# Kernel optimization log

Measured on AMD Instinct MI355X. Metric: run time of the kernel, lower is better.

Reference implementation:

```python
import jax, jax.numpy as jnp
import numpy as np

B, N, F, E, D, H, L = 4, 2048, 2, 16, 32, 4, 2
GRAPH_LAYERS = 3
FLOW_ITERS = 10
COST_C = 1.0        # quadratic cost: c*x^2, inv_derivative(y) = y/(2c)
BIG_NUMBER = 1e7


def setup_inputs():
    key = jax.random.key(0)
    ks = jax.random.split(key, 20)
    node_features = jax.random.normal(ks[0], (B, N, F), jnp.float32)
    node_embeddings = jax.random.normal(ks[1], (B, N, E), jnp.float32)
    demands = jax.random.normal(ks[2], (B, N, 1), jnp.float32)
    demands = demands - demands.mean(axis=1, keepdims=True)  # flow conservation
    adj = (jax.random.uniform(ks[3], (B, N, N)) < 0.01).astype(jnp.float32)
    adj = adj * (1.0 - jnp.eye(N, dtype=jnp.float32))
    eye = jnp.broadcast_to(jnp.eye(N, dtype=jnp.float32), (B, N, N))
    neighborhoods = jnp.stack([eye, adj], axis=1)  # [B,L,N,N] hop-0 and hop-1
    def g(k, shape):
        return jax.random.normal(k, shape, jnp.float32) * 0.1
    params = {
        'We1': g(ks[4], (E + F, D)), 'be1': jnp.zeros((D,), jnp.float32),
        'We2': g(ks[5], (D, D)), 'be2': jnp.zeros((D,), jnp.float32),
        'w_attn': g(ks[6], (H, D)),
        'Wo': g(ks[7], (D, D)), 'bo': jnp.zeros((D,), jnp.float32),
        'Wz': g(ks[8], (D, D)), 'Uz': g(ks[9], (D, D)), 'bz': jnp.zeros((D,), jnp.float32),
        'Wr': g(ks[10], (D, D)), 'Ur': g(ks[11], (D, D)), 'br': jnp.zeros((D,), jnp.float32),
        'Wh': g(ks[12], (D, D)), 'Uh': g(ks[13], (D, D)), 'bh': jnp.zeros((D,), jnp.float32),
        'Wd1': g(ks[14], (D, D)), 'bd1': jnp.zeros((D,), jnp.float32),
        'Wd2': g(ks[15], (D, 1)), 'bd2': jnp.zeros((1,), jnp.float32),
        'Wv1': g(ks[16], (D, D)), 'bv1': jnp.zeros((D,), jnp.float32),
        'Wv2': g(ks[17], (D, 1)), 'bv2': jnp.zeros((1,), jnp.float32),
    }
    return {'node_features': node_features, 'node_embeddings': node_embeddings,
            'demands': demands, 'adj': adj, 'neighborhoods': neighborhoods, **params}


def _forward(node_features, node_embeddings, demands, adj, neighborhoods,
             We1, be1, We2, be2, w_attn, Wo, bo,
             Wz, Uz, bz, Wr, Ur, br, Wh, Uh, bh,
             Wd1, bd1, Wd2, bd2, Wv1, bv1, Wv2, bv2):
    # --- node encoder MLP (tanh, activate_final=True) ---
    x = jnp.concatenate([node_embeddings, node_features], axis=-1)   # [B,N,E+F]
    enc = jnp.tanh(jnp.tanh(x @ We1 + be1) @ We2 + be2)               # [B,N,D]
    # row-normalized neighborhood operators (degree-normalized aggregation)
    Mnorm = neighborhoods / (jnp.sum(neighborhoods, axis=-1, keepdims=True) + 1.0)
    # --- graph_layers x (attention neighborhood + GRU state update) ---
    for _ in range(GRAPH_LAYERS):
        agg = jnp.einsum('blnm,bmd->blnd', Mnorm, enc)                # [B,L,N,D]
        scores = jnp.einsum('blnd,hd->bhnl', jnp.tanh(agg), w_attn)   # [B,H,N,L]
        alpha = jax.nn.softmax(scores, axis=-1)
        ctx = jnp.einsum('bhnl,blnd->bnd', alpha, agg) / H            # mean over heads
        nbr = jnp.tanh(ctx @ Wo + bo)                                 # [B,N,D]
        z = jax.nn.sigmoid(nbr @ Wz + enc @ Uz + bz)
        r = jax.nn.sigmoid(nbr @ Wr + enc @ Ur + br)
        h = jnp.tanh(nbr @ Wh + (r * enc) @ Uh + bh)
        enc = z * enc + (1.0 - z) * h
    # --- primal: edge weights, masked softmax, proportional flow solver ---
    pred = (enc @ Wd1 + bd1) @ Wd2 + bd2                              # [B,N,1]
    pw = pred * jnp.transpose(pred, (0, 2, 1))                        # [B,N,N]
    weights = -BIG_NUMBER * (1.0 - adj) + pw
    fwp = jax.nn.softmax(weights, axis=-1)                            # rows sum to 1
    flow0 = fwp * jax.nn.relu(-demands)

    def step(flow, _):
        inflow = jnp.sum(flow, axis=1)[..., None]                     # [B,N,1]
        return fwp * jax.nn.relu(inflow - demands), None

    flow, _ = jax.lax.scan(step, flow0, None, length=FLOW_ITERS)
    flow_cost = jnp.sum(COST_C * flow * flow, axis=(1, 2))            # [B]
    # --- dual: dual variables, dual flows via inverse cost derivative ---
    dual = (enc @ Wv1 + bv1) @ Wv2 + bv2                              # [B,N,1]
    dd = dual - jnp.transpose(dual, (0, 2, 1))                        # [B,N,N]
    df = adj * jax.nn.relu(dd / (2.0 * COST_C))
    dual_cost = jnp.sum(COST_C * df * df - dd * df, axis=(1, 2)) \
        - jnp.sum(dual * demands, axis=(1, 2))                        # [B]
    return flow_cost - dual_cost                                      # primal-dual gap loss, [B]


def reference(node_features, node_embeddings, demands, adj, neighborhoods,
              We1, be1, We2, be2, w_attn, Wo, bo,
              Wz, Uz, bz, Wr, Ur, br, Wh, Uh, bh,
              Wd1, bd1, Wd2, bd2, Wv1, bv1, Wv2, bv2):
    return _forward(node_features, node_embeddings, demands, adj, neighborhoods,
                    We1, be1, We2, be2, w_attn, Wo, bo,
                    Wz, Uz, bz, Wr, Ur, br, Wh, Uh, bh,
                    Wd1, bd1, Wd2, bd2, Wv1, bv1, Wv2, bv2)
```

## Files before the change

### kernel.cpp

```cpp
#include <hip/hip_runtime.h>

#define NN 2048
#define NB 4
#define BN (NB * NN)
#define MAXD 96

__global__ __launch_bounds__(256) void k_front(
    const float* __restrict__ feat, const float* __restrict__ emb,
    const float* __restrict__ We1, const float* __restrict__ be1,
    const float* __restrict__ We2, const float* __restrict__ be2,
    float* __restrict__ enc_out,
    const float* __restrict__ adj, int* __restrict__ deg, int* __restrict__ cols,
    int* __restrict__ tdeg)
{
    int tid = threadIdx.x;
    if (blockIdx.x < 1024) {
        __shared__ float sW1[18 * 32], sb1[32], sW2[32 * 32], sb2[32];
        for (int i = tid; i < 18 * 32; i += 256) sW1[i] = We1[i];
        for (int i = tid; i < 32 * 32; i += 256) sW2[i] = We2[i];
        if (tid < 32) { sb1[tid] = be1[tid]; sb2[tid] = be2[tid]; }
        __syncthreads();
        int group = tid >> 5, j = tid & 31;
        int node = blockIdx.x * 8 + group;
        float x;
        if (j < 16)      x = emb[node * 16 + j];
        else if (j < 18) x = feat[node * 2 + (j - 16)];
        else             x = 0.f;
        float acc = sb1[j];
#pragma unroll
        for (int k = 0; k < 18; k++)
            acc += __shfl(x, k, 32) * sW1[k * 32 + j];
        float h = tanhf(acc);
        float acc2 = sb2[j];
#pragma unroll
        for (int k = 0; k < 32; k++)
            acc2 += __shfl(h, k, 32) * sW2[k * 32 + j];
        enc_out[node * 32 + j] = tanhf(acc2);
    } else {
        int wave = tid >> 6, lane = tid & 63;
        int row = (blockIdx.x - 1024) * 4 + wave;
        const float4* p = (const float4*)(adj + (size_t)row * NN);
        int cnt = 0;
        int base = row * MAXD;
#pragma unroll
        for (int it = 0; it < 8; it++) {
            float4 v = p[it * 64 + lane];
            float va[4] = { v.x, v.y, v.z, v.w };
#pragma unroll
            for (int c = 0; c < 4; c++) {
                unsigned long long m = __ballot(va[c] != 0.f);
                if (va[c] != 0.f) {
                    int pos = cnt + __popcll(m & ((1ull << lane) - 1ull));
                    if (pos < MAXD) cols[base + pos] = it * 256 + lane * 4 + c;
                }
                cnt += __popcll(m);
            }
        }
        if (lane == 0) {
            deg[row] = cnt < MAXD ? cnt : MAXD;
            tdeg[row] = 0;
        }
    }
}

__global__ __launch_bounds__(256) void k_layer(
    const float* __restrict__ enc_in, float* __restrict__ enc_out,
    const int* __restrict__ deg, const int* __restrict__ cols,
    const float* __restrict__ w_attn,
    const float* __restrict__ Wo, const float* __restrict__ bo,
    const float* __restrict__ Wz, const float* __restrict__ Uz, const float* __restrict__ bz,
    const float* __restrict__ Wr, const float* __restrict__ Ur, const float* __restrict__ br,
    const float* __restrict__ Wh, const float* __restrict__ Uh, const float* __restrict__ bh)
{
    __shared__ float sWo[1024], sWz[1024], sUz[1024], sWr[1024], sUr[1024], sWh[1024], sUh[1024];
    __shared__ float sbo[32], sbz[32], sbr[32], sbh[32], sAttn[128];
    int tid = threadIdx.x;
    for (int i = tid; i < 1024; i += 256) {
        sWo[i] = Wo[i]; sWz[i] = Wz[i]; sUz[i] = Uz[i];
        sWr[i] = Wr[i]; sUr[i] = Ur[i]; sWh[i] = Wh[i]; sUh[i] = Uh[i];
    }
    if (tid < 32) { sbo[tid] = bo[tid]; sbz[tid] = bz[tid]; sbr[tid] = br[tid]; sbh[tid] = bh[tid]; }
    if (tid < 128) sAttn[tid] = w_attn[tid];
    __syncthreads();
    int group = tid >> 5, j = tid & 31;
    int node = blockIdx.x * 8 + group;
    int b = node >> 11;
    const float* encB = enc_in + (size_t)(b * NN) * 32;
    float e = enc_in[node * 32 + j];
    float agg0 = 0.5f * e;
    int d = deg[node];
    const int* cp = cols + node * MAXD;
    int iA = cp[j];
    int iB = cp[j + 32];
    float a1 = 0.f, a1b = 0.f;
    int dmin = d < 32 ? d : 32;
#pragma unroll 4
    for (int i = 0; i < dmin - 1; i += 2) {
        int m0 = __shfl(iA, i, 32);
        int m1 = __shfl(iA, i + 1, 32);
        a1  += encB[m0 * 32 + j];
        a1b += encB[m1 * 32 + j];
    }
    if (dmin & 1) { int m = __shfl(iA, dmin - 1, 32); a1 += encB[m * 32 + j]; }
#pragma unroll 2
    for (int i = 32; i < d; i++) {
        int m = __shfl(iB, i - 32, 32);
        a1 += encB[m * 32 + j];
    }
    a1 = (a1 + a1b) * (1.0f / (float)(d + 1));
    float t0 = tanhf(agg0), t1 = tanhf(a1);
    float sc[8];
#pragma unroll
    for (int h2 = 0; h2 < 4; h2++) { sc[h2] = sAttn[h2 * 32 + j] * t0; sc[4 + h2] = sAttn[h2 * 32 + j] * t1; }
#pragma unroll
    for (int off = 16; off >= 1; off >>= 1)
#pragma unroll
        for (int q = 0; q < 8; q++) sc[q] += __shfl_xor(sc[q], off, 32);
    float c0 = 0.f, c1 = 0.f;
#pragma unroll
    for (int h2 = 0; h2 < 4; h2++) {
        float a = sc[h2], bsc = sc[4 + h2];
        float mx = fmaxf(a, bsc);
        float e0 = expf(a - mx), e1 = expf(bsc - mx);
        float inv = 1.0f / (e0 + e1);
        c0 += e0 * inv; c1 += e1 * inv;
    }
    c0 *= 0.25f; c1 *= 0.25f;
    float ctx = c0 * agg0 + c1 * a1;
    float acc = sbo[j];
#pragma unroll
    for (int k = 0; k < 32; k++) acc += __shfl(ctx, k, 32) * sWo[k * 32 + j];
    float nbr = tanhf(acc);
    float az = sbz[j], ar = sbr[j], ah = sbh[j];
#pragma unroll
    for (int k = 0; k < 32; k++) {
        float nb = __shfl(nbr, k, 32);
        float en = __shfl(e, k, 32);
        az += nb * sWz[k * 32 + j] + en * sUz[k * 32 + j];
        ar += nb * sWr[k * 32 + j] + en * sUr[k * 32 + j];
        ah += nb * sWh[k * 32 + j];
    }
    float z = 1.0f / (1.0f + expf(-az));
    float r = 1.0f / (1.0f + expf(-ar));
    float re = r * e;
#pragma unroll
    for (int k = 0; k < 32; k++) ah += __shfl(re, k, 32) * sUh[k * 32 + j];
    float hc = tanhf(ah);
    enc_out[node * 32 + j] = z * e + (1.0f - z) * hc;
}

__global__ __launch_bounds__(256) void k_heads(
    const float* __restrict__ enc,
    const float* __restrict__ Wd1, const float* __restrict__ bd1,
    const float* __restrict__ Wd2, const float* __restrict__ bd2,
    const float* __restrict__ Wv1, const float* __restrict__ bv1,
    const float* __restrict__ Wv2, const float* __restrict__ bv2,
    float* __restrict__ pred, float* __restrict__ dual)
{
    __shared__ float sWd1[1024], sWv1[1024], sbd1[32], sbv1[32], sWd2[32], sWv2[32];
    int tid = threadIdx.x;
    for (int i = tid; i < 1024; i += 256) { sWd1[i] = Wd1[i]; sWv1[i] = Wv1[i]; }
    if (tid < 32) { sbd1[tid] = bd1[tid]; sbv1[tid] = bv1[tid]; sWd2[tid] = Wd2[tid]; sWv2[tid] = Wv2[tid]; }
    __syncthreads();
    int group = tid >> 5, j = tid & 31;
    int node = blockIdx.x * 8 + group;
    float e = enc[node * 32 + j];
    float ad = sbd1[j], av = sbv1[j];
#pragma unroll
    for (int k = 0; k < 32; k++) {
        float en = __shfl(e, k, 32);
        ad += en * sWd1[k * 32 + j];
        av += en * sWv1[k * 32 + j];
    }
    float pd = ad * sWd2[j];
    float dv = av * sWv2[j];
#pragma unroll
    for (int off = 16; off >= 1; off >>= 1) {
        pd += __shfl_xor(pd, off, 32);
        dv += __shfl_xor(dv, off, 32);
    }
    if (j == 0) {
        pred[node] = pd + bd2[0];
        dual[node] = dv + bv2[0];
    }
}

__global__ __launch_bounds__(256) void k_edge_scatter(
    const int* __restrict__ deg, const int* __restrict__ cols,
    const float* __restrict__ pred, const float* __restrict__ dual,
    int* __restrict__ tdeg, float2* __restrict__ pk,
    float* __restrict__ rowsq, float* __restrict__ rowdual)
{
    int wave = threadIdx.x >> 6, lane = threadIdx.x & 63;
    int row = blockIdx.x * 4 + wave;
    int b = row >> 11;
    int rloc = row & (NN - 1);
    const float* predB = pred + b * NN;
    const float* dualB = dual + b * NN;
    int d = deg[row];
    int base = row * MAXD;
    float pn = pred[row];
    float dn = dual[row];
    float mx = -1e30f;
    for (int i = lane; i < d; i += 64) {
        int c = cols[base + i];
        mx = fmaxf(mx, pn * predB[c]);
    }
#pragma unroll
    for (int off = 32; off >= 1; off >>= 1) mx = fmaxf(mx, __shfl_xor(mx, off));
    float den = 0.f, du = 0.f;
    for (int i = lane; i < d; i += 64) {
        int c = cols[base + i];
        den += expf(pn * predB[c] - mx);
        float dd = dn - dualB[c];
        if (dd > 0.f) du -= 0.25f * dd * dd;
    }
#pragma unroll
    for (int off = 32; off >= 1; off >>= 1) { den += __shfl_xor(den, off); du += __shfl_xor(du, off); }
    float invden = 1.0f / den;
    float rs = 0.f;
    for (int i = lane; i < d; i += 64) {
        int c = cols[base + i];
        float f = expf(pn * predB[c] - mx) * invden;
        rs += f * f;
        int pos = atomicAdd(&tdeg[b * NN + c], 1);
        if (pos < MAXD) {
            pk[((size_t)(b * NN) + c) * MAXD + pos] = make_float2(f, __int_as_float(rloc));
        }
    }
#pragma unroll
    for (int off = 32; off >= 1; off >>= 1) rs += __shfl_xor(rs, off);
    if (lane == 0) { rowsq[row] = rs; rowdual[row] = du; }
}

#define FLOW_GATHER(EPTR, PAIRS, REM, DTOT, SRC, ACC_A, ACC_B)                     \
    {                                                                              \
        int i_ = 0;                                                                \
        for (; i_ + 1 < (PAIRS); i_ += 2) {                                        \
            float4 qa_ = (EPTR)[i_];                                               \
            float4 qb_ = (EPTR)[i_ + 1];                                           \
            ACC_A += qa_.x * SRC[__float_as_int(qa_.y)];                           \
            ACC_B += qa_.z * SRC[__float_as_int(qa_.w)];                           \
            ACC_A += qb_.x * SRC[__float_as_int(qb_.y)];                           \
            ACC_B += qb_.z * SRC[__float_as_int(qb_.w)];                           \
        }                                                                          \
        if (i_ < (PAIRS)) {                                                        \
            float4 q_ = (EPTR)[i_];                                                \
            ACC_A += q_.x * SRC[__float_as_int(q_.y)];                             \
            ACC_B += q_.z * SRC[__float_as_int(q_.w)];                             \
        }                                                                          \
        if (REM) {                                                                 \
            float2 q_ = ((const float2*)(EPTR))[(DTOT) - 1];                       \
            ACC_A += q_.x * SRC[__float_as_int(q_.y)];                             \
        }                                                                          \
    }

__global__ __launch_bounds__(1024) void k_flow_batch(
    const int* __restrict__ tdeg, const float2* __restrict__ pk,
    const float* __restrict__ demands,
    const float* __restrict__ rowsq, const float* __restrict__ rowdual,
    const float* __restrict__ dual, float* __restrict__ out)
{
    __shared__ float sdem[NN], sA[NN], sBuf[NN];
    __shared__ float red[3][16];
    int tid = threadIdx.x;
    int b = blockIdx.x;
    const float* demB = demands + b * NN;
    for (int n = tid; n < NN; n += 1024) {
        float dm = demB[n];
        sdem[n] = dm;
        sA[n] = fmaxf(-dm, 0.f);
    }
    __syncthreads();
    int n0 = tid, n1 = tid + 1024;
    int d0 = tdeg[b * NN + n0];
    int d1 = tdeg[b * NN + n1];
    const float4* e0 = (const float4*)(pk + ((size_t)(b * NN) + n0) * MAXD);
    const float4* e1 = (const float4*)(pk + ((size_t)(b * NN) + n1) * MAXD);
    int p0 = d0 >> 1, r0 = d0 & 1;
    int p1 = d1 >> 1, r1 = d1 & 1;
    float dm0 = sdem[n0], dm1 = sdem[n1];
#pragma unroll 1
    for (int it = 0; it < 5; it++) {
        {
            float a0 = 0.f, a0b = 0.f, a1 = 0.f, a1b = 0.f;
            FLOW_GATHER(e0, p0, r0, d0, sA, a0, a0b);
            FLOW_GATHER(e1, p1, r1, d1, sA, a1, a1b);
            sBuf[n0] = fmaxf(a0 + a0b - dm0, 0.f);
            sBuf[n1] = fmaxf(a1 + a1b - dm1, 0.f);
        }
        __syncthreads();
        {
            float a0 = 0.f, a0b = 0.f, a1 = 0.f, a1b = 0.f;
            FLOW_GATHER(e0, p0, r0, d0, sBuf, a0, a0b);
            FLOW_GATHER(e1, p1, r1, d1, sBuf, a1, a1b);
            sA[n0] = fmaxf(a0 + a0b - dm0, 0.f);
            sA[n1] = fmaxf(a1 + a1b - dm1, 0.f);
        }
        __syncthreads();
    }
    float fc = 0.f, ds = 0.f, dq = 0.f;
    for (int n = tid; n < NN; n += 1024) {
        int row = b * NN + n;
        float sv = sA[n];
        fc += rowsq[row] * sv * sv;
        ds += rowdual[row];
        dq += dual[row] * sdem[n];
    }
#pragma unroll
    for (int off = 32; off >= 1; off >>= 1) {
        fc += __shfl_xor(fc, off);
        ds += __shfl_xor(ds, off);
        dq += __shfl_xor(dq, off);
    }
    int wv = tid >> 6;
    if ((tid & 63) == 0) { red[0][wv] = fc; red[1][wv] = ds; red[2][wv] = dq; }
    __syncthreads();
    if (tid == 0) {
        float a = 0.f, s1 = 0.f, s2 = 0.f;
        for (int w = 0; w < 16; w++) { a += red[0][w]; s1 += red[1][w]; s2 += red[2][w]; }
        out[b] = a - s1 + s2;
    }
}

extern "C" void kernel_launch(void* const* d_in, const int* in_sizes, int n_in,
                              void* d_out, int out_size, void* d_ws, size_t ws_size,
                              hipStream_t stream) {
    const float* feat = (const float*)d_in[0];
    const float* emb  = (const float*)d_in[1];
    const float* dem  = (const float*)d_in[2];
    const float* adj  = (const float*)d_in[3];
    const float* We1 = (const float*)d_in[5];
    const float* be1 = (const float*)d_in[6];
    const float* We2 = (const float*)d_in[7];
    const float* be2 = (const float*)d_in[8];
    const float* w_attn = (const float*)d_in[9];
    const float* Wo = (const float*)d_in[10];
    const float* bo = (const float*)d_in[11];
    const float* Wz = (const float*)d_in[12];
    const float* Uz = (const float*)d_in[13];
    const float* bz = (const float*)d_in[14];
    const float* Wr = (const float*)d_in[15];
    const float* Ur = (const float*)d_in[16];
    const float* br = (const float*)d_in[17];
    const float* Wh = (const float*)d_in[18];
    const float* Uh = (const float*)d_in[19];
    const float* bh = (const float*)d_in[20];
    const float* Wd1 = (const float*)d_in[21];
    const float* bd1 = (const float*)d_in[22];
    const float* Wd2 = (const float*)d_in[23];
    const float* bd2 = (const float*)d_in[24];
    const float* Wv1 = (const float*)d_in[25];
    const float* bv1 = (const float*)d_in[26];
    const float* Wv2 = (const float*)d_in[27];
    const float* bv2 = (const float*)d_in[28];
    float* out = (float*)d_out;

    float* w = (float*)d_ws;
    float* enc0 = w;            w += (size_t)BN * 32;
    float* enc1 = w;            w += (size_t)BN * 32;
    int*   degp = (int*)w;      w += BN;
    int*   colp = (int*)w;      w += (size_t)BN * MAXD;
    float* pred = w;            w += BN;
    float* dual = w;            w += BN;
    float* rowsq = w;           w += BN;
    float* rowdual = w;         w += BN;
    int*   tdeg = (int*)w;      w += BN;
    float2* pk = (float2*)w;    w += (size_t)BN * MAXD * 2;

    k_front<<<3072, 256, 0, stream>>>(feat, emb, We1, be1, We2, be2, enc0,
                                      adj, degp, colp, tdeg);
    k_layer<<<BN / 8, 256, 0, stream>>>(enc0, enc1, degp, colp, w_attn,
                                        Wo, bo, Wz, Uz, bz, Wr, Ur, br, Wh, Uh, bh);
    k_layer<<<BN / 8, 256, 0, stream>>>(enc1, enc0, degp, colp, w_attn,
                                        Wo, bo, Wz, Uz, bz, Wr, Ur, br, Wh, Uh, bh);
    k_layer<<<BN / 8, 256, 0, stream>>>(enc0, enc1, degp, colp, w_attn,
                                        Wo, bo, Wz, Uz, bz, Wr, Ur, br, Wh, Uh, bh);
    k_heads<<<BN / 8, 256, 0, stream>>>(enc1, Wd1, bd1, Wd2, bd2, Wv1, bv1, Wv2, bv2,
                                        pred, dual);
    k_edge_scatter<<<BN / 4, 256, 0, stream>>>(degp, colp, pred, dual,
                                               tdeg, pk, rowsq, rowdual);
    k_flow_batch<<<NB, 1024, 0, stream>>>(tdeg, pk, dem,
                                          rowsq, rowdual, dual, out);
}
```

Baseline: 476.3 us.

## Transpose flow edge buffer to slot-major layout and enlarge layer blocks

New measurement: 435.9 us. -8.5%, faster.

```diff
diff --git a/kernel.cpp b/kernel.cpp
--- a/kernel.cpp
+++ b/kernel.cpp
@@ -63,7 +63,7 @@
     }
 }
 
-__global__ __launch_bounds__(256) void k_layer(
+__global__ __launch_bounds__(1024) void k_layer(
     const float* __restrict__ enc_in, float* __restrict__ enc_out,
     const int* __restrict__ deg, const int* __restrict__ cols,
     const float* __restrict__ w_attn,
@@ -75,7 +75,8 @@
     __shared__ float sWo[1024], sWz[1024], sUz[1024], sWr[1024], sUr[1024], sWh[1024], sUh[1024];
     __shared__ float sbo[32], sbz[32], sbr[32], sbh[32], sAttn[128];
     int tid = threadIdx.x;
-    for (int i = tid; i < 1024; i += 256) {
+    {
+        int i = tid;
         sWo[i] = Wo[i]; sWz[i] = Wz[i]; sUz[i] = Uz[i];
         sWr[i] = Wr[i]; sUr[i] = Ur[i]; sWh[i] = Wh[i]; sUh[i] = Uh[i];
     }
@@ -83,7 +84,7 @@
     if (tid < 128) sAttn[tid] = w_attn[tid];
     __syncthreads();
     int group = tid >> 5, j = tid & 31;
-    int node = blockIdx.x * 8 + group;
+    int node = blockIdx.x * 32 + group;
     int b = node >> 11;
     const float* encB = enc_in + (size_t)(b * NN) * 32;
     float e = enc_in[node * 32 + j];
@@ -225,35 +226,13 @@
         rs += f * f;
         int pos = atomicAdd(&tdeg[b * NN + c], 1);
         if (pos < MAXD) {
-            pk[((size_t)(b * NN) + c) * MAXD + pos] = make_float2(f, __int_as_float(rloc));
+            pk[(size_t)(b * MAXD + pos) * NN + c] = make_float2(f, __int_as_float(rloc));
         }
     }
 #pragma unroll
     for (int off = 32; off >= 1; off >>= 1) rs += __shfl_xor(rs, off);
     if (lane == 0) { rowsq[row] = rs; rowdual[row] = du; }
 }
-
-#define FLOW_GATHER(EPTR, PAIRS, REM, DTOT, SRC, ACC_A, ACC_B)                     \
-    {                                                                              \
-        int i_ = 0;                                                                \
-        for (; i_ + 1 < (PAIRS); i_ += 2) {                                        \
-            float4 qa_ = (EPTR)[i_];                                               \
-            float4 qb_ = (EPTR)[i_ + 1];                                           \
-            ACC_A += qa_.x * SRC[__float_as_int(qa_.y)];                           \
-            ACC_B += qa_.z * SRC[__float_as_int(qa_.w)];                           \
-            ACC_A += qb_.x * SRC[__float_as_int(qb_.y)];                           \
-            ACC_B += qb_.z * SRC[__float_as_int(qb_.w)];                           \
-        }                                                                          \
-        if (i_ < (PAIRS)) {                                                        \
-            float4 q_ = (EPTR)[i_];                                                \
-            ACC_A += q_.x * SRC[__float_as_int(q_.y)];                             \
-            ACC_B += q_.z * SRC[__float_as_int(q_.w)];                             \
-        }                                                                          \
-        if (REM) {                                                                 \
-            float2 q_ = ((const float2*)(EPTR))[(DTOT) - 1];                       \
-            ACC_A += q_.x * SRC[__float_as_int(q_.y)];                             \
-        }                                                                          \
-    }
 
 __global__ __launch_bounds__(1024) void k_flow_batch(
     const int* __restrict__ tdeg, const float2* __restrict__ pk,
@@ -275,25 +254,55 @@
     int n0 = tid, n1 = tid + 1024;
     int d0 = tdeg[b * NN + n0];
     int d1 = tdeg[b * NN + n1];
-    const float4* e0 = (const float4*)(pk + ((size_t)(b * NN) + n0) * MAXD);
-    const float4* e1 = (const float4*)(pk + ((size_t)(b * NN) + n1) * MAXD);
-    int p0 = d0 >> 1, r0 = d0 & 1;
-    int p1 = d1 >> 1, r1 = d1 & 1;
+    const float2* e0 = pk + (size_t)b * MAXD * NN + n0;
+    const float2* e1 = pk + (size_t)b * MAXD * NN + n1;
     float dm0 = sdem[n0], dm1 = sdem[n1];
 #pragma unroll 1
     for (int it = 0; it < 5; it++) {
         {
             float a0 = 0.f, a0b = 0.f, a1 = 0.f, a1b = 0.f;
-            FLOW_GATHER(e0, p0, r0, d0, sA, a0, a0b);
-            FLOW_GATHER(e1, p1, r1, d1, sA, a1, a1b);
+            int i = 0;
+#pragma unroll 2
+            for (; i + 1 < d0; i += 2) {
+                float2 qa = e0[(size_t)i * NN];
+                float2 qb = e0[(size_t)(i + 1) * NN];
+                a0  += qa.x * sA[__float_as_int(qa.y)];
+                a0b += qb.x * sA[__float_as_int(qb.y)];
+            }
+            if (i < d0) { float2 q = e0[(size_t)i * NN]; a0 += q.x * sA[__float_as_int(q.y)]; }
+            i = 0;
+#pragma unroll 2
+            for (; i + 1 < d1; i += 2) {
+                float2 qa = e1[(size_t)i * NN];
+                float2 qb = e1[(size_t)(i + 1) * NN];
+                a1  += qa.x * sA[__float_as_int(qa.y)];
+                a1b += qb.x * sA[__float_as_int(qb.y)];
+            }
+            if (i < d1) { float2 q = e1[(size_t)i * NN]; a1 += q.x * sA[__float_as_int(q.y)]; }
             sBuf[n0] = fmaxf(a0 + a0b - dm0, 0.f);
             sBuf[n1] = fmaxf(a1 + a1b - dm1, 0.f);
         }
         __syncthreads();
         {
             float a0 = 0.f, a0b = 0.f, a1 = 0.f, a1b = 0.f;
-            FLOW_GATHER(e0, p0, r0, d0, sBuf, a0, a0b);
-            FLOW_GATHER(e1, p1, r1, d1, sBuf, a1, a1b);
+            int i = 0;
+#pragma unroll 2
+            for (; i + 1 < d0; i += 2) {
+                float2 qa = e0[(size_t)i * NN];
+                float2 qb = e0[(size_t)(i + 1) * NN];
+                a0  += qa.x * sBuf[__float_as_int(qa.y)];
+                a0b += qb.x * sBuf[__float_as_int(qb.y)];
+            }
+            if (i < d0) { float2 q = e0[(size_t)i * NN]; a0 += q.x * sBuf[__float_as_int(q.y)]; }
+            i = 0;
+#pragma unroll 2
+            for (; i + 1 < d1; i += 2) {
+                float2 qa = e1[(size_t)i * NN];
+                float2 qb = e1[(size_t)(i + 1) * NN];
+                a1  += qa.x * sBuf[__float_as_int(qa.y)];
+                a1b += qb.x * sBuf[__float_as_int(qb.y)];
+            }
+            if (i < d1) { float2 q = e1[(size_t)i * NN]; a1 += q.x * sBuf[__float_as_int(q.y)]; }
             sA[n0] = fmaxf(a0 + a0b - dm0, 0.f);
             sA[n1] = fmaxf(a1 + a1b - dm1, 0.f);
         }
@@ -370,12 +379,12 @@
 
     k_front<<<3072, 256, 0, stream>>>(feat, emb, We1, be1, We2, be2, enc0,
                                       adj, degp, colp, tdeg);
-    k_layer<<<BN / 8, 256, 0, stream>>>(enc0, enc1, degp, colp, w_attn,
-                                        Wo, bo, Wz, Uz, bz, Wr, Ur, br, Wh, Uh, bh);
-    k_layer<<<BN / 8, 256, 0, stream>>>(enc1, enc0, degp, colp, w_attn,
-                                        Wo, bo, Wz, Uz, bz, Wr, Ur, br, Wh, Uh, bh);
-    k_layer<<<BN / 8, 256, 0, stream>>>(enc0, enc1, degp, colp, w_attn,
-                                        Wo, bo, Wz, Uz, bz, Wr, Ur, br, Wh, Uh, bh);
+    k_layer<<<BN / 32, 1024, 0, stream>>>(enc0, enc1, degp, colp, w_attn,
+                                          Wo, bo, Wz, Uz, bz, Wr, Ur, br, Wh, Uh, bh);
+    k_layer<<<BN / 32, 1024, 0, stream>>>(enc1, enc0, degp, colp, w_attn,
+                                          Wo, bo, Wz, Uz, bz, Wr, Ur, br, Wh, Uh, bh);
+    k_layer<<<BN / 32, 1024, 0, stream>>>(enc0, enc1, degp, colp, w_attn,
+                                          Wo, bo, Wz, Uz, bz, Wr, Ur, br, Wh, Uh, bh);
     k_heads<<<BN / 8, 256, 0, stream>>>(enc1, Wd1, bd1, Wd2, bd2, Wv1, bv1, Wv2, bv2,
                                         pred, dual);
     k_edge_scatter<<<BN / 4, 256, 0, stream>>>(degp, colp, pred, dual,
```

## Store transposed flow edges column-major and widen layer blocks to 1024 threads

Applied to the files above, without the earlier changes.

Measured after the change: 456.6 us. 4.1% less time.

```diff
diff --git a/kernel.cpp b/kernel.cpp
--- a/kernel.cpp
+++ b/kernel.cpp
@@ -63,7 +63,7 @@
     }
 }
 
-__global__ __launch_bounds__(256) void k_layer(
+__global__ __launch_bounds__(1024) void k_layer(
     const float* __restrict__ enc_in, float* __restrict__ enc_out,
     const int* __restrict__ deg, const int* __restrict__ cols,
     const float* __restrict__ w_attn,
@@ -75,7 +75,8 @@
     __shared__ float sWo[1024], sWz[1024], sUz[1024], sWr[1024], sUr[1024], sWh[1024], sUh[1024];
     __shared__ float sbo[32], sbz[32], sbr[32], sbh[32], sAttn[128];
     int tid = threadIdx.x;
-    for (int i = tid; i < 1024; i += 256) {
+    {
+        int i = tid;
         sWo[i] = Wo[i]; sWz[i] = Wz[i]; sUz[i] = Uz[i];
         sWr[i] = Wr[i]; sUr[i] = Ur[i]; sWh[i] = Wh[i]; sUh[i] = Uh[i];
     }
@@ -83,7 +84,7 @@
     if (tid < 128) sAttn[tid] = w_attn[tid];
     __syncthreads();
     int group = tid >> 5, j = tid & 31;
-    int node = blockIdx.x * 8 + group;
+    int node = blockIdx.x * 32 + group;
     int b = node >> 11;
     const float* encB = enc_in + (size_t)(b * NN) * 32;
     float e = enc_in[node * 32 + j];
@@ -188,7 +189,7 @@
 __global__ __launch_bounds__(256) void k_edge_scatter(
     const int* __restrict__ deg, const int* __restrict__ cols,
     const float* __restrict__ pred, const float* __restrict__ dual,
-    int* __restrict__ tdeg, float2* __restrict__ pk,
+    int* __restrict__ tdeg, int* __restrict__ tcols, float* __restrict__ tvals,
     float* __restrict__ rowsq, float* __restrict__ rowdual)
 {
     int wave = threadIdx.x >> 6, lane = threadIdx.x & 63;
@@ -225,7 +226,9 @@
         rs += f * f;
         int pos = atomicAdd(&tdeg[b * NN + c], 1);
         if (pos < MAXD) {
-            pk[((size_t)(b * NN) + c) * MAXD + pos] = make_float2(f, __int_as_float(rloc));
+            size_t idx = (size_t)(b * MAXD + pos) * NN + c;
+            tcols[idx] = rloc;
+            tvals[idx] = f;
         }
     }
 #pragma unroll
@@ -233,31 +236,29 @@
     if (lane == 0) { rowsq[row] = rs; rowdual[row] = du; }
 }
 
-#define FLOW_GATHER(EPTR, PAIRS, REM, DTOT, SRC, ACC_A, ACC_B)                     \
+#define GATH8(TC, TV, D, SRC, ACCA, ACCB)                                          \
     {                                                                              \
         int i_ = 0;                                                                \
-        for (; i_ + 1 < (PAIRS); i_ += 2) {                                        \
-            float4 qa_ = (EPTR)[i_];                                               \
-            float4 qb_ = (EPTR)[i_ + 1];                                           \
-            ACC_A += qa_.x * SRC[__float_as_int(qa_.y)];                           \
-            ACC_B += qa_.z * SRC[__float_as_int(qa_.w)];                           \
-            ACC_A += qb_.x * SRC[__float_as_int(qb_.y)];                           \
-            ACC_B += qb_.z * SRC[__float_as_int(qb_.w)];                           \
+        for (; i_ + 8 <= (D); i_ += 8) {                                           \
+            float vv_[8]; int ss_[8];                                              \
+            _Pragma("unroll")                                                      \
+            for (int k_ = 0; k_ < 8; k_++) {                                       \
+                vv_[k_] = (TV)[(size_t)(i_ + k_) * NN];                            \
+                ss_[k_] = (TC)[(size_t)(i_ + k_) * NN];                            \
+            }                                                                      \
+            _Pragma("unroll")                                                      \
+            for (int k_ = 0; k_ < 8; k_ += 2) {                                    \
+                ACCA += vv_[k_] * SRC[ss_[k_]];                                    \
+                ACCB += vv_[k_ + 1] * SRC[ss_[k_ + 1]];                            \
+            }                                                                      \
         }                                                                          \
-        if (i_ < (PAIRS)) {                                                        \
-            float4 q_ = (EPTR)[i_];                                                \
-            ACC_A += q_.x * SRC[__float_as_int(q_.y)];                             \
-            ACC_B += q_.z * SRC[__float_as_int(q_.w)];                             \
-        }                                                                          \
-        if (REM) {                                                                 \
-            float2 q_ = ((const float2*)(EPTR))[(DTOT) - 1];                       \
-            ACC_A += q_.x * SRC[__float_as_int(q_.y)];                             \
-        }                                                                          \
+        for (; i_ < (D); i_++)                                                     \
+            ACCA += (TV)[(size_t)i_ * NN] * SRC[(TC)[(size_t)i_ * NN]];            \
     }
 
 __global__ __launch_bounds__(1024) void k_flow_batch(
-    const int* __restrict__ tdeg, const float2* __restrict__ pk,
-    const float* __restrict__ demands,
+    const int* __restrict__ tdeg, const int* __restrict__ tcols,
+    const float* __restrict__ tvals, const float* __restrict__ demands,
     const float* __restrict__ rowsq, const float* __restrict__ rowdual,
     const float* __restrict__ dual, float* __restrict__ out)
 {
@@ -275,25 +276,25 @@
     int n0 = tid, n1 = tid + 1024;
     int d0 = tdeg[b * NN + n0];
     int d1 = tdeg[b * NN + n1];
-    const float4* e0 = (const float4*)(pk + ((size_t)(b * NN) + n0) * MAXD);
-    const float4* e1 = (const float4*)(pk + ((size_t)(b * NN) + n1) * MAXD);
-    int p0 = d0 >> 1, r0 = d0 & 1;
-    int p1 = d1 >> 1, r1 = d1 & 1;
+    const int*   tc0 = tcols + (size_t)b * MAXD * NN + n0;
+    const float* tv0 = tvals + (size_t)b * MAXD * NN + n0;
+    const int*   tc1 = tcols + (size_t)b * MAXD * NN + n1;
+    const float* tv1 = tvals + (size_t)b * MAXD * NN + n1;
     float dm0 = sdem[n0], dm1 = sdem[n1];
 #pragma unroll 1
     for (int it = 0; it < 5; it++) {
         {
             float a0 = 0.f, a0b = 0.f, a1 = 0.f, a1b = 0.f;
-            FLOW_GATHER(e0, p0, r0, d0, sA, a0, a0b);
-            FLOW_GATHER(e1, p1, r1, d1, sA, a1, a1b);
+            GATH8(tc0, tv0, d0, sA, a0, a0b);
+            GATH8(tc1, tv1, d1, sA, a1, a1b);
             sBuf[n0] = fmaxf(a0 + a0b - dm0, 0.f);
             sBuf[n1] = fmaxf(a1 + a1b - dm1, 0.f);
         }
         __syncthreads();
         {
             float a0 = 0.f, a0b = 0.f, a1 = 0.f, a1b = 0.f;
-            FLOW_GATHER(e0, p0, r0, d0, sBuf, a0, a0b);
-            FLOW_GATHER(e1, p1, r1, d1, sBuf, a1, a1b);
+            GATH8(tc0, tv0, d0, sBuf, a0, a0b);
+            GATH8(tc1, tv1, d1, sBuf, a1, a1b);
             sA[n0] = fmaxf(a0 + a0b - dm0, 0.f);
             sA[n1] = fmaxf(a1 + a1b - dm1, 0.f);
         }
@@ -366,20 +367,21 @@
     float* rowsq = w;           w += BN;
     float* rowdual = w;         w += BN;
     int*   tdeg = (int*)w;      w += BN;
-    float2* pk = (float2*)w;    w += (size_t)BN * MAXD * 2;
+    int*   tcol = (int*)w;      w += (size_t)BN * MAXD;
+    float* tval = w;            w += (size_t)BN * MAXD;
 
     k_front<<<3072, 256, 0, stream>>>(feat, emb, We1, be1, We2, be2, enc0,
                                       adj, degp, colp, tdeg);
-    k_layer<<<BN / 8, 256, 0, stream>>>(enc0, enc1, degp, colp, w_attn,
-                                        Wo, bo, Wz, Uz, bz, Wr, Ur, br, Wh, Uh, bh);
-    k_layer<<<BN / 8, 256, 0, stream>>>(enc1, enc0, degp, colp, w_attn,
-                                        Wo, bo, Wz, Uz, bz, Wr, Ur, br, Wh, Uh, bh);
-    k_layer<<<BN / 8, 256, 0, stream>>>(enc0, enc1, degp, colp, w_attn,
-                                        Wo, bo, Wz, Uz, bz, Wr, Ur, br, Wh, Uh, bh);
+    k_layer<<<BN / 32, 1024, 0, stream>>>(enc0, enc1, degp, colp, w_attn,
+                                          Wo, bo, Wz, Uz, bz, Wr, Ur, br, Wh, Uh, bh);
+    k_layer<<<BN / 32, 1024, 0, stream>>>(enc1, enc0, degp, colp, w_attn,
+                                          Wo, bo, Wz, Uz, bz, Wr, Ur, br, Wh, Uh, bh);
+    k_layer<<<BN / 32, 1024, 0, stream>>>(enc0, enc1, degp, colp, w_attn,
+                                          Wo, bo, Wz, Uz, bz, Wr, Ur, br, Wh, Uh, bh);
     k_heads<<<BN / 8, 256, 0, stream>>>(enc1, Wd1, bd1, Wd2, bd2, Wv1, bv1, Wv2, bv2,
                                         pred, dual);
     k_edge_scatter<<<BN / 4, 256, 0, stream>>>(degp, colp, pred, dual,
-                                               tdeg, pk, rowsq, rowdual);
-    k_flow_batch<<<NB, 1024, 0, stream>>>(tdeg, pk, dem,
+                                               tdeg, tcol, tval, rowsq, rowdual);
+    k_flow_batch<<<NB, 1024, 0, stream>>>(tdeg, tcol, tval, dem,
                                           rowsq, rowdual, dual, out);
 }
```
